# Optimization experiments

Measured on AMD Instinct MI355X. Metric: run time of the kernel, lower is better.

## Reference

```python
import jax, jax.numpy as jnp
import numpy as np

NG, SNG, NS, SNS, NR = 4, 2, 4, 2, 3
NW = 4
STEP = 1 + NG + SNG + NS + SNS + NR  # 16
T, D = 512, 64
MARGIN, ALPHA, BETA, P, R = 1.0, 0.01, 1.0, 0.1, 0.1
KNUM, KMUL = 5, 2.0
GAMMA = 5.0          # soft-dtw gamma
BIG = 1e9            # finite 'inf' so softmin grads stay NaN-free
SIZ = NW * (NW + 1) // 2  # mmds buffer size in the original (zero padded)


def setup_inputs() -> dict:
    key = jax.random.key(0)
    k1, k2 = jax.random.split(key)
    data = jax.random.normal(k1, (NW * STEP, T, D), dtype=jnp.float32)
    lens = jax.random.randint(k2, (NW * STEP,), 64, T + 1, dtype=jnp.int32)
    return {"data": data, "lens": lens}


def _softdtw(Dmat, la, lb):
    """Soft-DTW via anti-diagonal scan. Dmat: (T,T) squared-euclid costs.
    Returns R[la, lb]; DP cells only depend on smaller indices so padding is inert."""
    Tn = Dmat.shape[0]
    idx = jnp.arange(Tn)

    def step(carry, k):
        r2, r1 = carry                      # diagonals k-2 and k-1, indexed by i
        j = k - idx
        valid = (j >= 0) & (j < Tn)
        d = jnp.where(valid, Dmat[idx, jnp.clip(j, 0, Tn - 1)], BIG)
        up = jnp.where(idx > 0, jnp.roll(r1, 1), BIG)     # cell (i-1, j)
        left = r1                                          # cell (i, j-1)
        diag = jnp.where(idx > 0, jnp.roll(r2, 1), BIG)    # cell (i-1, j-1)
        diag = jnp.where((idx == 0) & (k == 0), 0.0, diag)  # R[0,0] = 0 border
        m = jnp.stack([diag, up, left])
        softmin = -GAMMA * jax.nn.logsumexp(-m / GAMMA, axis=0)
        r = jnp.where(valid, d + softmin, BIG)
        return (r1, r), r

    init = (jnp.full((Tn,), BIG, Dmat.dtype), jnp.full((Tn,), BIG, Dmat.dtype))
    _, rows = jax.lax.scan(step, init, jnp.arange(2 * Tn - 1))
    # rows[k, i] = R[i+1, k-i+1]; want R[la, lb] -> k = la+lb-2, i = la-1
    return rows[la + lb - 2, la - 1]


def _mmd(x, y):
    """Multi-kernel Gaussian MMD (DAN-style MMDLoss), n == m."""
    n = x.shape[0]
    total = jnp.concatenate([x, y], axis=0)          # (2n, F)
    sq = jnp.sum(total * total, axis=1)
    l2 = sq[:, None] + sq[None, :] - 2.0 * (total @ total.T)
    ns = total.shape[0]
    bw = jnp.sum(l2) / (ns * ns - ns)
    bw = bw / (KMUL ** (KNUM // 2))
    bws = bw * (KMUL ** jnp.arange(KNUM, dtype=total.dtype))
    kern = jnp.sum(jnp.exp(-l2[None] / bws[:, None, None]), axis=0)
    XX, YY, XY, YX = kern[:n, :n], kern[n:, n:], kern[:n, n:], kern[n:, :n]
    return jnp.mean(XX + YY - XY - YX)


def _forward(data, lens):
    d = data.reshape(NW, STEP, T, D)
    li = lens.reshape(NW, STEP)
    Lf = li.astype(data.dtype)
    anchors = d[:, 0]          # (nw, T, D)
    others = d[:, 1:]          # (nw, 15, T, D)

    # squared-euclidean cost matrices via GEMM: (nw, 15, T, T)
    a2 = jnp.sum(anchors * anchors, -1)                      # (nw, T)
    b2 = jnp.sum(others * others, -1)                        # (nw, 15, T)
    ab = jnp.einsum('wtd,wjsd->wjts', anchors, others)
    cost = a2[:, None, :, None] + b2[:, :, None, :] - 2.0 * ab

    laB = jnp.broadcast_to(li[:, :1], (NW, STEP - 1))
    sdt = jax.vmap(jax.vmap(_softdtw))(cost, laB, li[:, 1:])  # (nw, 15)
    dist = sdt / (Lf[:, :1] + Lf[:, 1:])

    dist_g = dist[:, :NG + SNG]    # genuine + synthetic genuine (6)
    dist_n = dist[:, NG + SNG:]    # skilled + syn skilled + random (9)

    lk = jax.nn.relu(dist_g[:, :, None] + MARGIN - dist_n[:, None, :])
    ca = jnp.mean(dist_g, axis=1)
    cb = jnp.mean(dist_n[:, :5], axis=1)
    intra = jnp.sum(dist_g - ca[:, None], axis=1)
    inter = jax.nn.relu(BETA - jnp.abs(ca - cb))
    nz = jnp.sum(lk != 0, axis=(1, 2))
    lv = jnp.sum(lk, axis=(1, 2)) / (nz + 1).astype(data.dtype)
    total_loss = jnp.mean(lv + intra * P + inter * R)

    # MMD over all (i, j) pairs written by the original loop (i in 0..nw-1,
    # j in 1..nw-1, i != j); buffer zero-padded to SIZ, then max * alpha.
    groups = d[:, :STEP - 5].reshape(NW, STEP - 5, T * D)
    pi = jnp.array([0, 0, 0, 1, 1, 2, 2, 3, 3])
    pj = jnp.array([1, 2, 3, 2, 3, 1, 3, 1, 2])
    mmds = jax.vmap(_mmd)(groups[pi], groups[pj])
    mmds = jnp.concatenate([mmds, jnp.zeros((SIZ - pi.shape[0],), data.dtype)])
    mmd1 = jnp.max(mmds) * ALPHA
    return total_loss + mmd1


def reference(data, lens):
    return _forward(data, lens)
```

## Files before the change

### kernel.cpp

```cpp
#include <hip/hip_runtime.h>
#include <hip/hip_bf16.h>

#define TT   512
#define DD   64
#define NWK  4
#define STP  16
#define NPJ  15
#define NBLK 60
#define CMAT (TT * TT)
#define CSCALE 0.2885390081777927f
#define USCALE 3.4657359027997265f
#define BIGC   2.885390081777927e8f

#define SWZ(k) (((((k) >> 2) & 7)) << 2)

__global__ __launch_bounds__(256, 1) void cost_kernel(const float* __restrict__ data,
                                                      const int* __restrict__ lens,
                                                      float* __restrict__ cost, int base) {
  int blk = base + blockIdx.z;
  int w = blk / NPJ, j = blk - w * NPJ;
  int la = lens[w * STP];
  int lb = lens[w * STP + 1 + j];
  int ti = blockIdx.y, tj = blockIdx.x;
  if (ti * 128 >= la || tj * 128 >= lb) return;

  __shared__ float As[DD][128];
  __shared__ float Bs[DD][128];
  __shared__ float a2[128], b2[128];

  const float* A = data + ((size_t)(w * STP) * TT + (size_t)ti * 128) * DD;
  const float* B = data + ((size_t)(w * STP + 1 + j) * TT + (size_t)tj * 128) * DD;
  int t = threadIdx.x;

  #pragma unroll
  for (int i = 0; i < 8; ++i) {
    int f = t + i * 256;
    int r = f >> 4;
    int k0 = (f & 15) << 2;
    int cs = r ^ SWZ(k0);
    float4 va = *(const float4*)(A + r * DD + k0);
    As[k0 + 0][cs] = va.x; As[k0 + 1][cs] = va.y;
    As[k0 + 2][cs] = va.z; As[k0 + 3][cs] = va.w;
    float4 vb = *(const float4*)(B + r * DD + k0);
    Bs[k0 + 0][cs] = vb.x; Bs[k0 + 1][cs] = vb.y;
    Bs[k0 + 2][cs] = vb.z; Bs[k0 + 3][cs] = vb.w;
  }
  __syncthreads();
  if (t < 128) {
    float s = 0.f;
    #pragma unroll 8
    for (int k = 0; k < DD; ++k) { float x = As[k][t ^ SWZ(k)]; s += x * x; }
    a2[t] = s;
  } else {
    int u = t - 128;
    float s = 0.f;
    #pragma unroll 8
    for (int k = 0; k < DD; ++k) { float x = Bs[k][u ^ SWZ(k)]; s += x * x; }
    b2[u] = s;
  }
  __syncthreads();

  int r0 = (t >> 4) << 2;
  int c0 = (t & 15) << 2;
  float acc[8][8];
  #pragma unroll
  for (int i = 0; i < 8; ++i)
    #pragma unroll
    for (int q = 0; q < 8; ++q) acc[i][q] = 0.f;

  float4 aL = *(const float4*)&As[0][r0];
  float4 aH = *(const float4*)&As[0][r0 + 64];
  float4 bL = *(const float4*)&Bs[0][c0];
  float4 bH = *(const float4*)&Bs[0][c0 + 64];

  #pragma unroll 4
  for (int k = 0; k < DD; ++k) {
    int kn = (k + 1) & 63;
    int sw = SWZ(kn);
    float4 naL = *(const float4*)&As[kn][r0 ^ sw];
    float4 naH = *(const float4*)&As[kn][(r0 + 64) ^ sw];
    float4 nbL = *(const float4*)&Bs[kn][c0 ^ sw];
    float4 nbH = *(const float4*)&Bs[kn][(c0 + 64) ^ sw];
    float a[8] = {aL.x, aL.y, aL.z, aL.w, aH.x, aH.y, aH.z, aH.w};
    float b[8] = {bL.x, bL.y, bL.z, bL.w, bH.x, bH.y, bH.z, bH.w};
    #pragma unroll
    for (int i = 0; i < 8; ++i)
      #pragma unroll
      for (int q = 0; q < 8; ++q)
        acc[i][q] += a[i] * b[q];
    aL = naL; aH = naH; bL = nbL; bH = nbH;
  }

  float* Cbase = cost + (size_t)blockIdx.z * CMAT;
  #pragma unroll
  for (int i = 0; i < 8; ++i) {
    int rr = (i < 4) ? (r0 + i) : (r0 + 60 + i);
    float ar = a2[rr];
    float* Crow = Cbase + (size_t)(ti * 128 + rr) * TT + tj * 128;
    float4 o;
    o.x = (ar + b2[c0 + 0] - 2.f * acc[i][0]) * CSCALE;
    o.y = (ar + b2[c0 + 1] - 2.f * acc[i][1]) * CSCALE;
    o.z = (ar + b2[c0 + 2] - 2.f * acc[i][2]) * CSCALE;
    o.w = (ar + b2[c0 + 3] - 2.f * acc[i][3]) * CSCALE;
    *(float4*)(Crow + c0) = o;
    float4 o2;
    o2.x = (ar + b2[c0 + 64] - 2.f * acc[i][4]) * CSCALE;
    o2.y = (ar + b2[c0 + 65] - 2.f * acc[i][5]) * CSCALE;
    o2.z = (ar + b2[c0 + 66] - 2.f * acc[i][6]) * CSCALE;
    o2.w = (ar + b2[c0 + 67] - 2.f * acc[i][7]) * CSCALE;
    *(float4*)(Crow + c0 + 64) = o2;
  }
}

__device__ __forceinline__ float dpcell(float dc, float a, float b, float c) {
  float mn = fminf(fminf(a, b), c);
  float mx = fmaxf(fmaxf(a, b), c);
  float md = __builtin_amdgcn_fmed3f(a, b, c);
  float e = 1.0f + __builtin_amdgcn_exp2f(mn - md) + __builtin_amdgcn_exp2f(mn - mx);
  return dc + mn - __builtin_amdgcn_logf(e);
}

#define LDNXT(kk, gg)                                                         \
  { int rr = 8 * ((gg) + 1) + (kk) - ln;                                      \
    rr = rr < 0 ? 0 : (rr > 511 ? 511 : rr);                                  \
    nxt[kk] = *(const float2*)(Cp + (size_t)rr * TT); }

#define DPSTEP(kk, gg)                                                        \
  {                                                                           \
    int r = 8 * (gg) + (kk) - ln;                                             \
    if ((unsigned)r < 512u) {                                                 \
      float v0 = dpcell(cur[kk].x, NLd, U0, NL);                              \
      float v1 = dpcell(cur[kk].y, U0, U1, v0);                               \
      if (isT & (r == rt)) res = par ? v1 : v0;                               \
      NLd = NL; U0 = v0; U1 = v1; v1s = v1;                                   \
      if (wr63) {                                                             \
        bufB[q][r] = v1;                                                      \
        if ((r & 7) == 7) {                                                   \
          asm volatile("s_waitcnt lgkmcnt(0)" ::: "memory");   \
          *(volatile int*)&flags[q] = r + 1;                                  \
        }                                                                     \
      }                                                                       \
    }                                                                         \
    float nb = __shfl_up(v1s, 1);                                             \
    if (ln == 0) nb = (q == 0) ? BIGC : bb[kk];                               \
    NL = nb;                                                                  \
  }

#define DPGROUP(gg)                                                           \
  {                                                                           \
    LDNXT(0, gg) LDNXT(1, gg) LDNXT(2, gg) LDNXT(3, gg)                       \
    LDNXT(4, gg) LDNXT(5, gg) LDNXT(6, gg) LDNXT(7, gg)                       \
    __builtin_amdgcn_sched_barrier(0);          \
    if (q > 0) {                                                              \
      int need = 8 * (gg) + 9; if (need > la) need = la;                      \
      while (*(volatile int*)&flags[q - 1] < need) __builtin_amdgcn_s_sleep(1); \
      asm volatile("" ::: "memory");      \
      bb[0] = bufB[q - 1][8 * (gg) + 1]; bb[1] = bufB[q - 1][8 * (gg) + 2];   \
      bb[2] = bufB[q - 1][8 * (gg) + 3]; bb[3] = bufB[q - 1][8 * (gg) + 4];   \
      bb[4] = bufB[q - 1][8 * (gg) + 5]; bb[5] = bufB[q - 1][8 * (gg) + 6];   \
      bb[6] = bufB[q - 1][8 * (gg) + 7]; bb[7] = bufB[q - 1][8 * (gg) + 8];   \
    }                                                                         \
    DPSTEP(0, gg) DPSTEP(1, gg) DPSTEP(2, gg) DPSTEP(3, gg)                   \
    DPSTEP(4, gg) DPSTEP(5, gg) DPSTEP(6, gg) DPSTEP(7, gg)                   \
    cur[0] = nxt[0]; cur[1] = nxt[1]; cur[2] = nxt[2]; cur[3] = nxt[3];       \
    cur[4] = nxt[4]; cur[5] = nxt[5]; cur[6] = nxt[6]; cur[7] = nxt[7];       \
  }

__global__ __launch_bounds__(256, 1) void dp_gram_kernel(const float* __restrict__ cost,
                                                         const int* __restrict__ lens,
                                                         const float* __restrict__ data,
                                                         float* __restrict__ sdt,
                                                         float* __restrict__ gram,
                                                         int base, int ndp) {
  int bid = blockIdx.x;

  if (bid >= ndp) {
    __shared__ float red[4][16];
    int g = bid - ndp;
    int bx = g / 11, by = g - bx * 11;
    int t = threadIdx.x;
    const float* Ar[4]; const float* Br[4];
    #pragma unroll
    for (int a = 0; a < 4; ++a) {
      int gx = bx * 4 + a;
      Ar[a] = data + (size_t)((gx / 11) * STP + gx % 11) * (TT * DD);
      int gy = by * 4 + a;
      Br[a] = data + (size_t)((gy / 11) * STP + gy % 11) * (TT * DD);
    }
    float acc[4][4];
    #pragma unroll
    for (int a = 0; a < 4; ++a)
      #pragma unroll
      for (int b = 0; b < 4; ++b) acc[a][b] = 0.f;
    for (int k = t * 4; k < TT * DD; k += 1024) {
      float4 av[4], bv[4];
      #pragma unroll
      for (int a = 0; a < 4; ++a) av[a] = *(const float4*)(Ar[a] + k);
      #pragma unroll
      for (int b = 0; b < 4; ++b) bv[b] = *(const float4*)(Br[b] + k);
      #pragma unroll
      for (int a = 0; a < 4; ++a)
        #pragma unroll
        for (int b = 0; b < 4; ++b)
          acc[a][b] += av[a].x * bv[b].x + av[a].y * bv[b].y +
                       av[a].z * bv[b].z + av[a].w * bv[b].w;
    }
    int wave = t >> 6, lane = t & 63;
    #pragma unroll
    for (int a = 0; a < 4; ++a)
      #pragma unroll
      for (int b = 0; b < 4; ++b) {
        float v = acc[a][b];
        for (int off = 32; off > 0; off >>= 1) v += __shfl_down(v, off);
        if (lane == 0) red[wave][a * 4 + b] = v;
      }
    __syncthreads();
    if (t < 16) {
      float v = red[0][t] + red[1][t] + red[2][t] + red[3][t];
      int a = t >> 2, b = t & 3;
      gram[(size_t)(bx * 4 + a) * 44 + by * 4 + b] = v;
    }
    return;
  }

  __shared__ float bufB[3][640];
  __shared__ int flags[4];

  if (threadIdx.x < 4) flags[threadIdx.x] = 0;
  __syncthreads();

  int blk = base + bid;
  int w = blk / NPJ, j = blk - w * NPJ;
  int la = lens[w * STP];
  int lb = lens[w * STP + 1 + j];
  const float* C = cost + (size_t)bid * CMAT;

  int q = threadIdx.x >> 6, ln = threadIdx.x & 63;
  int c0 = q * 128 + ln * 2;
  const float* Cp = C + c0;
  bool wr63 = (q < 3) & (ln == 63);

  int qt = (lb - 1) >> 7;
  int lt = ((lb - 1) >> 1) & 63;
  int par = (lb - 1) & 1;
  int rt = la - 1;
  bool isT = (q == qt) && (ln == lt);

  float U0 = BIGC, U1 = BIGC;
  float NL = BIGC;
  float NLd = (q == 0 && ln == 0) ? 0.0f : BIGC;
  float v1s = BIGC;
  float res = 0.0f;
  float bb[8];

  int ngrp = (la + 70) >> 3;

  float2 cur[8], nxt[8];
  #pragma unroll
  for (int k = 0; k < 8; ++k) {
    int rr = k - ln; rr = rr < 0 ? 0 : rr;
    cur[k] = *(const float2*)(Cp + (size_t)rr * TT);
  }

  for (int g = 0; g < ngrp; ++g) {
    DPGROUP(g)
  }
  if (wr63) {
    asm volatile("s_waitcnt lgkmcnt(0)" ::: "memory");
    *(volatile int*)&flags[q] = 512;
  }
  if (isT) sdt[blk] = res * USCALE;
}

__global__ __launch_bounds__(640) void final_kernel(const float* __restrict__ sdt,
                                                    const int* __restrict__ lens,
                                                    const float* __restrict__ gram,
                                                    float* __restrict__ out) {
  __shared__ float partial[16];
  int t = threadIdx.x, wave = t >> 6, lane = t & 63;
  if (wave < 9) {
    const int piA[9] = {0, 0, 0, 1, 1, 2, 2, 3, 3};
    const int pjA[9] = {1, 2, 3, 2, 3, 1, 3, 1, 2};
    int P = piA[wave], Q = pjA[wave];
    float s1 = 0.f;
    for (int c = lane; c < 484; c += 64) {
      int i = c / 22, jj = c - (c / 22) * 22;
      int gi = (i < 11) ? P * 11 + i : Q * 11 + (i - 11);
      int gj = (jj < 11) ? P * 11 + jj : Q * 11 + (jj - 11);
      s1 += gram[gi * 44 + gi] + gram[gj * 44 + gj] - 2.f * gram[gi * 44 + gj];
    }
    for (int off = 32; off > 0; off >>= 1) s1 += __shfl_down(s1, off);
    s1 = __shfl(s1, 0);
    float bw = s1 / 462.0f * 0.25f;
    float inv[5];
    float b = bw;
    #pragma unroll
    for (int qq = 0; qq < 5; ++qq) { inv[qq] = -1.0f / b; b *= 2.0f; }
    float s2 = 0.f;
    for (int c = lane; c < 484; c += 64) {
      int i = c / 22, jj = c - (c / 22) * 22;
      int gi = (i < 11) ? P * 11 + i : Q * 11 + (i - 11);
      int gj = (jj < 11) ? P * 11 + jj : Q * 11 + (jj - 11);
      float l2 = gram[gi * 44 + gi] + gram[gj * 44 + gj] - 2.f * gram[gi * 44 + gj];
      float kk = 0.f;
      #pragma unroll
      for (int qq = 0; qq < 5; ++qq) kk += __expf(l2 * inv[qq]);
      float sgn = ((i < 11) == (jj < 11)) ? 1.0f : -1.0f;
      s2 += sgn * kk;
    }
    for (int off = 32; off > 0; off >>= 1) s2 += __shfl_down(s2, off);
    if (lane == 0) partial[wave] = s2 / 121.0f;
  } else {
    float term = 0.f;
    if (wave == 9 && lane < 4) {
      int w = lane;
      float L0 = (float)lens[w * STP];
      float dist[15];
      for (int qq = 0; qq < 15; ++qq)
        dist[qq] = sdt[w * NPJ + qq] / (L0 + (float)lens[w * STP + 1 + qq]);
      float ca = 0.f, cb = 0.f;
      for (int a = 0; a < 6; ++a) ca += dist[a];
      ca *= (1.0f / 6.0f);
      for (int bq = 6; bq < 11; ++bq) cb += dist[bq];
      cb *= (1.0f / 5.0f);
      float lksum = 0.f; int nz = 0;
      for (int a = 0; a < 6; ++a)
        for (int bq = 6; bq < 15; ++bq) {
          float x = dist[a] + 1.0f - dist[bq];
          if (x > 0.f) { lksum += x; nz += 1; }
        }
      float intra = 0.f;
      for (int a = 0; a < 6; ++a) intra += dist[a] - ca;
      float inter = fmaxf(0.f, 1.0f - fabsf(ca - cb));
      term = lksum / (float)(nz + 1) + intra * 0.1f + inter * 0.1f;
    }
    if (wave == 9) {
      term += __shfl_down(term, 1);
      term += __shfl_down(term, 2);
      if (lane == 0) partial[9] = term * 0.25f;
    }
  }
  __syncthreads();
  if (t == 0) {
    float mx = 0.0f;
    for (int p = 0; p < 9; ++p) mx = fmaxf(mx, partial[p]);
    out[0] = partial[9] + 0.01f * mx;
  }
}

extern "C" void kernel_launch(void* const* d_in, const int* in_sizes, int n_in,
                              void* d_out, int out_size, void* d_ws, size_t ws_size,
                              hipStream_t stream) {
  const float* data = (const float*)d_in[0];
  const int* lens = (const int*)d_in[1];
  float* out = (float*)d_out;

  float* sdtb  = (float*)d_ws;
  float* gramb = sdtb + 64;
  float* costb = (float*)((char*)d_ws + 8192);

  size_t avail = (ws_size > 8192) ? (ws_size - 8192) : 0;
  int chunk = (int)(avail / ((size_t)CMAT * sizeof(float)));
  if (chunk < 1) chunk = 1;
  if (chunk > NBLK) chunk = NBLK;

  bool first = true;
  for (int base = 0; base < NBLK; base += chunk) {
    int n = NBLK - base;
    if (n > chunk) n = chunk;
    cost_kernel<<<dim3(4, 4, n), 256, 0, stream>>>(data, lens, costb, base);
    int extra = first ? 121 : 0;
    dp_gram_kernel<<<n + extra, 256, 0, stream>>>(costb, lens, data, sdtb, gramb, base, n);
    first = false;
  }
  final_kernel<<<1, 640, 0, stream>>>(sdtb, lens, gramb, out);
}
```

Before: 242.0 us.

## Store cost matrix in skewed diagonal layout for coalesced DP loads

The cost kernel now writes cost values in a skewed, pair-interleaved layout, so each DP lane's anti-diagonal cells sit contiguously in one row of a compact buffer. The DP kernel then loads one float4 per lane per row pair instead of eight strided float2 loads across full rows. This should cut scattered global traffic and the buffer footprint, which may allow larger chunks. The cost is scattered float2 stores in the cost kernel and more complex indexing that has to match exactly between producer and consumer.

```diff
diff --git a/kernel.cpp b/kernel.cpp
--- a/kernel.cpp
+++ b/kernel.cpp
@@ -7,7 +7,8 @@
 #define STP  16
 #define NPJ  15
 #define NBLK 60
-#define CMAT (TT * TT)
+#define TROWS 304
+#define TSLOT (TROWS * TT)
 #define CSCALE 0.2885390081777927f
 #define USCALE 3.4657359027997265f
 #define BIGC   2.885390081777927e8f
@@ -16,7 +17,7 @@
 
 __global__ __launch_bounds__(256, 1) void cost_kernel(const float* __restrict__ data,
                                                       const int* __restrict__ lens,
-                                                      float* __restrict__ cost, int base) {
+                                                      float* __restrict__ costT, int base) {
   int blk = base + blockIdx.z;
   int w = blk / NPJ, j = blk - w * NPJ;
   int la = lens[w * STP];
@@ -91,24 +92,38 @@
     aL = naL; aH = naH; bL = nbL; bH = nbH;
   }
 
-  float* Cbase = cost + (size_t)blockIdx.z * CMAT;
+  float* Tb = costT + (size_t)blockIdx.z * TSLOT;
+  int ph = c0 >> 1;
+  int pbase = tj * 64 + ph;
   #pragma unroll
   for (int i = 0; i < 8; ++i) {
     int rr = (i < 4) ? (r0 + i) : (r0 + 60 + i);
+    int row = ti * 128 + rr;
     float ar = a2[rr];
-    float* Crow = Cbase + (size_t)(ti * 128 + rr) * TT + tj * 128;
-    float4 o;
-    o.x = (ar + b2[c0 + 0] - 2.f * acc[i][0]) * CSCALE;
-    o.y = (ar + b2[c0 + 1] - 2.f * acc[i][1]) * CSCALE;
-    o.z = (ar + b2[c0 + 2] - 2.f * acc[i][2]) * CSCALE;
-    o.w = (ar + b2[c0 + 3] - 2.f * acc[i][3]) * CSCALE;
-    *(float4*)(Crow + c0) = o;
-    float4 o2;
-    o2.x = (ar + b2[c0 + 64] - 2.f * acc[i][4]) * CSCALE;
-    o2.y = (ar + b2[c0 + 65] - 2.f * acc[i][5]) * CSCALE;
-    o2.z = (ar + b2[c0 + 66] - 2.f * acc[i][6]) * CSCALE;
-    o2.w = (ar + b2[c0 + 67] - 2.f * acc[i][7]) * CSCALE;
-    *(float4*)(Crow + c0 + 64) = o2;
+    {
+      int u = row + ph;
+      float2 o = { (ar + b2[c0 + 0] - 2.f * acc[i][0]) * CSCALE,
+                   (ar + b2[c0 + 1] - 2.f * acc[i][1]) * CSCALE };
+      *(float2*)(Tb + (size_t)(u >> 1) * TT + (pbase + 0) * 4 + (u & 1) * 2) = o;
+    }
+    {
+      int u = row + ph + 1;
+      float2 o = { (ar + b2[c0 + 2] - 2.f * acc[i][2]) * CSCALE,
+                   (ar + b2[c0 + 3] - 2.f * acc[i][3]) * CSCALE };
+      *(float2*)(Tb + (size_t)(u >> 1) * TT + (pbase + 1) * 4 + (u & 1) * 2) = o;
+    }
+    {
+      int u = row + ph + 32;
+      float2 o = { (ar + b2[c0 + 64] - 2.f * acc[i][4]) * CSCALE,
+                   (ar + b2[c0 + 65] - 2.f * acc[i][5]) * CSCALE };
+      *(float2*)(Tb + (size_t)(u >> 1) * TT + (pbase + 32) * 4 + (u & 1) * 2) = o;
+    }
+    {
+      int u = row + ph + 33;
+      float2 o = { (ar + b2[c0 + 66] - 2.f * acc[i][6]) * CSCALE,
+                   (ar + b2[c0 + 67] - 2.f * acc[i][7]) * CSCALE };
+      *(float2*)(Tb + (size_t)(u >> 1) * TT + (pbase + 33) * 4 + (u & 1) * 2) = o;
+    }
   }
 }
 
@@ -120,17 +135,14 @@
   return dc + mn - __builtin_amdgcn_logf(e);
 }
 
-#define LDNXT(kk, gg)                                                         \
-  { int rr = 8 * ((gg) + 1) + (kk) - ln;                                      \
-    rr = rr < 0 ? 0 : (rr > 511 ? 511 : rr);                                  \
-    nxt[kk] = *(const float2*)(Cp + (size_t)rr * TT); }
-
 #define DPSTEP(kk, gg)                                                        \
   {                                                                           \
     int r = 8 * (gg) + (kk) - ln;                                             \
+    float dx = ((kk) & 1) ? cur[(kk) >> 1].z : cur[(kk) >> 1].x;              \
+    float dy = ((kk) & 1) ? cur[(kk) >> 1].w : cur[(kk) >> 1].y;              \
     if ((unsigned)r < 512u) {                                                 \
-      float v0 = dpcell(cur[kk].x, NLd, U0, NL);                              \
-      float v1 = dpcell(cur[kk].y, U0, U1, v0);                               \
+      float v0 = dpcell(dx, NLd, U0, NL);                                     \
+      float v1 = dpcell(dy, U0, U1, v0);                                      \
       if (isT & (r == rt)) res = par ? v1 : v0;                               \
       NLd = NL; U0 = v0; U1 = v1; v1s = v1;                                   \
       if (wr63) {                                                             \
@@ -148,8 +160,10 @@
 
 #define DPGROUP(gg)                                                           \
   {                                                                           \
-    LDNXT(0, gg) LDNXT(1, gg) LDNXT(2, gg) LDNXT(3, gg)                       \
-    LDNXT(4, gg) LDNXT(5, gg) LDNXT(6, gg) LDNXT(7, gg)                       \
+    nxt[0] = *(const float4*)(Tp + (size_t)(4 * (gg) + 4) * TT);              \
+    nxt[1] = *(const float4*)(Tp + (size_t)(4 * (gg) + 5) * TT);              \
+    nxt[2] = *(const float4*)(Tp + (size_t)(4 * (gg) + 6) * TT);              \
+    nxt[3] = *(const float4*)(Tp + (size_t)(4 * (gg) + 7) * TT);              \
     __builtin_amdgcn_sched_barrier(0);          \
     if (q > 0) {                                                              \
       int need = 8 * (gg) + 9; if (need > la) need = la;                      \
@@ -163,15 +177,15 @@
     DPSTEP(0, gg) DPSTEP(1, gg) DPSTEP(2, gg) DPSTEP(3, gg)                   \
     DPSTEP(4, gg) DPSTEP(5, gg) DPSTEP(6, gg) DPSTEP(7, gg)                   \
     cur[0] = nxt[0]; cur[1] = nxt[1]; cur[2] = nxt[2]; cur[3] = nxt[3];       \
-    cur[4] = nxt[4]; cur[5] = nxt[5]; cur[6] = nxt[6]; cur[7] = nxt[7];       \
-  }
-
-__global__ __launch_bounds__(256, 1) void dp_gram_kernel(const float* __restrict__ cost,
-                                                         const int* __restrict__ lens,
-                                                         const float* __restrict__ data,
-                                                         float* __restrict__ sdt,
-                                                         float* __restrict__ gram,
-                                                         int base, int ndp) {
+  }
+
+__global__ __launch_bounds__(256, 1) __attribute__((amdgpu_waves_per_eu(1, 1)))
+void dp_gram_kernel(const float* __restrict__ costT,
+                    const int* __restrict__ lens,
+                    const float* __restrict__ data,
+                    float* __restrict__ sdt,
+                    float* __restrict__ gram,
+                    int base, int ndp) {
   int bid = blockIdx.x;
 
   if (bid >= ndp) {
@@ -233,15 +247,13 @@
   int w = blk / NPJ, j = blk - w * NPJ;
   int la = lens[w * STP];
   int lb = lens[w * STP + 1 + j];
-  const float* C = cost + (size_t)bid * CMAT;
 
   int q = threadIdx.x >> 6, ln = threadIdx.x & 63;
-  int c0 = q * 128 + ln * 2;
-  const float* Cp = C + c0;
+  const float* Tp = costT + (size_t)bid * TSLOT + (q * 64 + ln) * 4;
   bool wr63 = (q < 3) & (ln == 63);
 
   int qt = (lb - 1) >> 7;
-  int lt = ((lb - 1) >> 1) & 63;
+  int lt = ((lb - 1) & 127) >> 1;
   int par = (lb - 1) & 1;
   int rt = la - 1;
   bool isT = (q == qt) && (ln == lt);
@@ -255,12 +267,11 @@
 
   int ngrp = (la + 70) >> 3;
 
-  float2 cur[8], nxt[8];
-  #pragma unroll
-  for (int k = 0; k < 8; ++k) {
-    int rr = k - ln; rr = rr < 0 ? 0 : rr;
-    cur[k] = *(const float2*)(Cp + (size_t)rr * TT);
-  }
+  float4 cur[4], nxt[4];
+  cur[0] = *(const float4*)(Tp + (size_t)0 * TT);
+  cur[1] = *(const float4*)(Tp + (size_t)1 * TT);
+  cur[2] = *(const float4*)(Tp + (size_t)2 * TT);
+  cur[3] = *(const float4*)(Tp + (size_t)3 * TT);
 
   for (int g = 0; g < ngrp; ++g) {
     DPGROUP(g)
@@ -360,7 +371,7 @@
   float* costb = (float*)((char*)d_ws + 8192);
 
   size_t avail = (ws_size > 8192) ? (ws_size - 8192) : 0;
-  int chunk = (int)(avail / ((size_t)CMAT * sizeof(float)));
+  int chunk = (int)(avail / ((size_t)TSLOT * sizeof(float)));
   if (chunk < 1) chunk = 1;
   if (chunk > NBLK) chunk = NBLK;
 
```

New measurement: 255.0 us. 5.4% more time.
